# Optimization experiments

Measured on AMD Instinct MI355X. Metric: run time of the kernel, lower is better.

Reference implementation:

```python
import jax, jax.numpy as jnp
import numpy as np

EPS_MSG = 1e-7   # GENConv message epsilon
BN_EPS = 1e-5    # BatchNorm1d eps
NUM_GRAPHS = 1024


def _linear(x, W, b):
    return x @ W + b


def _batchnorm(x, gamma, beta):
    # training-mode batch statistics over the node dimension
    mu = jnp.mean(x, axis=0)
    var = jnp.mean((x - mu) ** 2, axis=0)
    return (x - mu) * jax.lax.rsqrt(var + BN_EPS) * gamma + beta


def _genconv(x, src, dst, e, t, W1, b1, gamma, beta, W2, b2, num_nodes):
    # message: relu(x_j + edge_attr) + eps, shape [E, H]
    msg = jax.nn.relu(x[src] + e) + EPS_MSG
    # learnable softmax aggregation over each destination's neighborhood
    s = msg * t
    m = jax.lax.stop_gradient(jax.ops.segment_max(s, dst, num_segments=num_nodes))
    m = jnp.where(jnp.isfinite(m), m, 0.0)
    ex = jnp.exp(s - m[dst])
    denom = jax.ops.segment_sum(ex, dst, num_segments=num_nodes)
    alpha = ex / (denom[dst] + 1e-16)
    agg = jax.ops.segment_sum(msg * alpha, dst, num_segments=num_nodes)  # [N, H]
    # GENConv MLP([H, 2H, H], norm='batch') applied to x + aggregated messages
    h = x + agg
    h = _linear(h, W1, b1)
    h = _batchnorm(h, gamma, beta)
    h = jax.nn.relu(h)
    return _linear(h, W2, b2)


def setup_inputs() -> dict:
    key = jax.random.key(0)
    N, E, FIN, FE, H, L, G, OUT = 50000, 1000000, 32, 16, 64, 4, NUM_GRAPHS, 1
    ks = jax.random.split(key, 32)

    def rn(k, shape, fan_in):
        return jax.random.normal(k, shape, dtype=jnp.float32) * (1.0 / np.sqrt(fan_in))

    inp = {}
    inp["x"] = jax.random.normal(ks[0], (N, FIN), dtype=jnp.float32)
    inp["edge_attr"] = jax.random.normal(ks[1], (E, FE), dtype=jnp.float32)
    inp["edge_index"] = jax.random.randint(ks[2], (2, E), 0, N)
    inp["batch"] = jnp.sort(jax.random.randint(ks[3], (N,), 0, G))
    # atom encoder: Linear(FIN,H) ReLU Linear(H,H) ReLU
    inp["atom_W1"] = rn(ks[4], (FIN, H), FIN); inp["atom_b1"] = jnp.zeros((H,), jnp.float32)
    inp["atom_W2"] = rn(ks[5], (H, H), H);     inp["atom_b2"] = jnp.zeros((H,), jnp.float32)
    # bond encoder: Linear(FE,H) ReLU Linear(H,H) ReLU
    inp["bond_W1"] = rn(ks[6], (FE, H), FE);   inp["bond_b1"] = jnp.zeros((H,), jnp.float32)
    inp["bond_W2"] = rn(ks[7], (H, H), H);     inp["bond_b2"] = jnp.zeros((H,), jnp.float32)
    # stacked GENConv params (L layers)
    inp["conv_t"] = jnp.ones((L,), jnp.float32)
    inp["conv_W1"] = rn(ks[8], (L, H, 2 * H), H)
    inp["conv_b1"] = jnp.zeros((L, 2 * H), jnp.float32)
    inp["conv_gamma"] = jnp.ones((L, 2 * H), jnp.float32)
    inp["conv_beta"] = jnp.zeros((L, 2 * H), jnp.float32)
    inp["conv_W2"] = rn(ks[9], (L, 2 * H, H), 2 * H)
    inp["conv_b2"] = jnp.zeros((L, H), jnp.float32)
    # head
    inp["lin1_W"] = rn(ks[10], (H, H), H);     inp["lin1_b"] = jnp.zeros((H,), jnp.float32)
    inp["lin2_W"] = rn(ks[11], (H, OUT), H);   inp["lin2_b"] = jnp.zeros((OUT,), jnp.float32)
    return inp


def reference(x, edge_attr, atom_W1, atom_b1, atom_W2, atom_b2,
              bond_W1, bond_b1, bond_W2, bond_b2,
              conv_t, conv_W1, conv_b1, conv_gamma, conv_beta, conv_W2, conv_b2,
              lin1_W, lin1_b, lin2_W, lin2_b,
              edge_index, batch):
    N = x.shape[0]
    src, dst = edge_index[0], edge_index[1]
    h = jax.nn.relu(_linear(jax.nn.relu(_linear(x, atom_W1, atom_b1)), atom_W2, atom_b2))
    e = jax.nn.relu(_linear(jax.nn.relu(_linear(edge_attr, bond_W1, bond_b1)), bond_W2, bond_b2))
    L = conv_t.shape[0]
    for i in range(L):
        h = _genconv(h, src, dst, e, conv_t[i], conv_W1[i], conv_b1[i],
                     conv_gamma[i], conv_beta[i], conv_W2[i], conv_b2[i], N)
        if i < L - 1:
            h = jax.nn.relu(h)
    g = jax.ops.segment_sum(h, batch, num_segments=NUM_GRAPHS)  # global_add_pool
    g = jax.nn.relu(_linear(g, lin1_W, lin1_b))
    return _linear(g, lin2_W, lin2_b)
```

## Files before the change

kernel.cpp:

```cpp
#include <hip/hip_runtime.h>
#include <hip/hip_bf16.h>
#include <math.h>

typedef __attribute__((ext_vector_type(8))) short bf16x8;
typedef __attribute__((ext_vector_type(4))) float f32x4;

__device__ inline unsigned f2bf(float f) {
    union { __hip_bfloat16 h; unsigned short u; } cv;
    cv.h = __float2bfloat16(f);
    return (unsigned)cv.u;
}
__device__ inline float bfu(unsigned u) {
    return __uint_as_float(u << 16);
}


__global__ void k_hist(const int* __restrict__ dst, int* __restrict__ counts, int E) {
    int e = blockIdx.x * blockDim.x + threadIdx.x;
    if (e < E) atomicAdd(&counts[dst[e]], 1);
}

__global__ void k_scan1(const int* __restrict__ counts, int* __restrict__ row_ptr,
                        int* __restrict__ csum, int n) {
    __shared__ int buf[1024];
    int tid = threadIdx.x;
    int base = blockIdx.x * 1024;
    int v = (base + tid < n) ? counts[base + tid] : 0;
    buf[tid] = v;
    __syncthreads();
    int inc = v;
    for (int off = 1; off < 1024; off <<= 1) {
        int add = (tid >= off) ? buf[tid - off] : 0;
        __syncthreads();
        inc += add;
        buf[tid] = inc;
        __syncthreads();
    }
    if (base + tid < n) row_ptr[base + tid] = inc - v;
    if (tid == 1023) csum[blockIdx.x] = inc;
}

__global__ void k_scan2(int* __restrict__ csum, int nc, int* __restrict__ total) {
    if (threadIdx.x == 0) {
        int run = 0;
        for (int i = 0; i < nc; ++i) { int c = csum[i]; csum[i] = run; run += c; }
        *total = run;
    }
}

__global__ void k_scan3(int* __restrict__ row_ptr, const int* __restrict__ csum,
                        const int* __restrict__ total, int n) {
    int i = blockIdx.x * blockDim.x + threadIdx.x;
    if (i < n) row_ptr[i] += csum[i >> 10];
    if (i == 0) row_ptr[n] = *total;
}

#define ECH 4096
__global__ __launch_bounds__(256) void k_scatter(const int* __restrict__ src,
                          const int* __restrict__ dst,
                          const int* __restrict__ row_ptr, int* __restrict__ fill,
                          int2* __restrict__ spe, int E, int NS) {
    int bs = blockIdx.x & 7;
    int chunk = blockIdx.x >> 3;
    int base = chunk * ECH;
    int lo = bs * NS, hi = lo + NS;
#pragma unroll 1
    for (int j = 0; j < ECH / 256; ++j) {
        int e = base + j * 256 + threadIdx.x;
        if (e < E) {
            int d = dst[e];
            if (d >= lo && d < hi) {
                int pos = row_ptr[d] + atomicAdd(&fill[d], 1);
                spe[pos] = make_int2(src[e], e);
            }
        }
    }
}

__global__ void k_gptr(const int* __restrict__ batch, int* __restrict__ gptr, int n, int G) {
    int i = blockIdx.x * blockDim.x + threadIdx.x;
    if (i > n) return;
    if (i == 0) {
        int b0 = batch[0];
        for (int g = 0; g <= b0; ++g) gptr[g] = 0;
    } else if (i == n) {
        int bl = batch[n - 1];
        for (int g = bl + 1; g <= G; ++g) gptr[g] = n;
    } else {
        int b = batch[i], pb = batch[i - 1];
        for (int g = pb + 1; g <= b; ++g) gptr[g] = i;
    }
}


__global__ void k_wt(const float* __restrict__ W1, const float* __restrict__ W2,
                     unsigned short* __restrict__ W1b, unsigned short* __restrict__ W2tb) {
    int tid = blockIdx.x * blockDim.x + threadIdx.x;
    if (tid < 1024) {
        int j = tid / 16, k = tid % 16;
        W1b[j * 16 + k] = (unsigned short)f2bf(W1[k * 64 + j]);
    }
    if (tid < 4096) {
        int j = tid / 64, k = tid % 64;
        W2tb[j * 64 + k] = (unsigned short)f2bf(W2[k * 64 + j]);
    }
}


#define TM 128
__global__ __launch_bounds__(256) void k_atom(const float* __restrict__ x,
        const float* __restrict__ W1, const float* __restrict__ b1,
        const float* __restrict__ W2, const float* __restrict__ b2,
        float* __restrict__ out, int M) {
    __shared__ float sU[TM * 65];
    __shared__ float sW1[32 * 64];
    __shared__ float sW2[64 * 64];
    __shared__ float sB1[64], sB2[64];
#define A_IN(r, c) sU[(r) * 33 + (c)]
#define A_T1(r, c) sU[(r) * 65 + (c)]
    int tid = threadIdx.x;
    int base = blockIdx.x * TM;
    for (int i = tid; i < 32 * 64 / 4; i += 256) ((float4*)sW1)[i] = ((const float4*)W1)[i];
    for (int i = tid; i < 64 * 64 / 4; i += 256) ((float4*)sW2)[i] = ((const float4*)W2)[i];
    if (tid < 64) { sB1[tid] = b1[tid]; sB2[tid] = b2[tid]; }
    for (int i = tid; i < TM * 32 / 4; i += 256) {
        int r = i / 8, c4 = i % 8;
        int row = base + r;
        float4 v = (row < M) ? ((const float4*)(x + (long)row * 32))[c4] : make_float4(0, 0, 0, 0);
        A_IN(r, c4 * 4 + 0) = v.x; A_IN(r, c4 * 4 + 1) = v.y;
        A_IN(r, c4 * 4 + 2) = v.z; A_IN(r, c4 * 4 + 3) = v.w;
    }
    __syncthreads();
    int r0 = (tid / 16) * 8;
    int c0 = (tid % 16) * 4;
    float acc[8][4];
#pragma unroll
    for (int i = 0; i < 8; i++)
#pragma unroll
        for (int j = 0; j < 4; j++) acc[i][j] = sB1[c0 + j];
    for (int k = 0; k < 32; k++) {
        float a[8], b[4];
#pragma unroll
        for (int i = 0; i < 8; i++) a[i] = A_IN(r0 + i, k);
#pragma unroll
        for (int j = 0; j < 4; j++) b[j] = sW1[k * 64 + c0 + j];
#pragma unroll
        for (int i = 0; i < 8; i++)
#pragma unroll
            for (int j = 0; j < 4; j++) acc[i][j] += a[i] * b[j];
    }
    __syncthreads();
#pragma unroll
    for (int i = 0; i < 8; i++)
#pragma unroll
        for (int j = 0; j < 4; j++) A_T1(r0 + i, c0 + j) = fmaxf(acc[i][j], 0.f);
    __syncthreads();
#pragma unroll
    for (int i = 0; i < 8; i++)
#pragma unroll
        for (int j = 0; j < 4; j++) acc[i][j] = sB2[c0 + j];
    for (int k = 0; k < 64; k++) {
        float a[8], b[4];
#pragma unroll
        for (int i = 0; i < 8; i++) a[i] = A_T1(r0 + i, k);
#pragma unroll
        for (int j = 0; j < 4; j++) b[j] = sW2[k * 64 + c0 + j];
#pragma unroll
        for (int i = 0; i < 8; i++)
#pragma unroll
            for (int j = 0; j < 4; j++) acc[i][j] += a[i] * b[j];
    }
#pragma unroll
    for (int i = 0; i < 8; i++) {
        int row = base + r0 + i;
        if (row < M) {
            float4 v = make_float4(fmaxf(acc[i][0], 0.f), fmaxf(acc[i][1], 0.f),
                                   fmaxf(acc[i][2], 0.f), fmaxf(acc[i][3], 0.f));
            *(float4*)(out + (long)row * 64 + c0) = v;
        }
    }
}


__global__ __launch_bounds__(256) void k_bond(const float* __restrict__ ea,
        const int2* __restrict__ spe,
        const unsigned short* __restrict__ W1b, const float* __restrict__ b1,
        const unsigned short* __restrict__ W2tb, const float* __restrict__ b2,
        unsigned short* __restrict__ e_q, int E) {
    __shared__ unsigned sT1[128 * 32];
    __shared__ unsigned sW2[64 * 32];
    int tid = threadIdx.x;

    for (int i = tid; i < 2048; i += 256) {
        int rw = i >> 5, cp = i & 31;
        sW2[rw * 32 + (cp ^ ((rw & 7) << 2))] = ((const unsigned*)W2tb)[i];
    }

    int wv = tid >> 6, lane = tid & 63;
    int lr = lane & 15, q = lane >> 4;

    union { bf16x8 v; uint4 u4; } bf1[4];
    float bias1[4];
#pragma unroll
    for (int nt = 0; nt < 4; ++nt) {
        bf1[nt].u4 = make_uint4(0, 0, 0, 0);
        if (q < 2)
            bf1[nt].u4 = *(const uint4*)(W1b + (nt * 16 + lr) * 16 + q * 8);
        bias1[nt] = b1[nt * 16 + lr];
    }

#pragma unroll
    for (int mt1 = 0; mt1 < 2; ++mt1) {
        int rtile = wv * 2 + mt1;
        long row1 = (long)blockIdx.x * 128 + rtile * 16 + lr;
        long eidx = row1 < (long)E ? row1 : (long)(E - 1);
        int eid = spe[eidx].y;
        union { bf16x8 v; uint4 u4; unsigned u[4]; } af1;
        af1.u4 = make_uint4(0, 0, 0, 0);
        if (q < 2) {
            const float4* er = (const float4*)(ea + (long)eid * 16 + q * 8);
            float4 u0 = er[0], u1 = er[1];
            af1.u[0] = f2bf(u0.x) | (f2bf(u0.y) << 16);
            af1.u[1] = f2bf(u0.z) | (f2bf(u0.w) << 16);
            af1.u[2] = f2bf(u1.x) | (f2bf(u1.y) << 16);
            af1.u[3] = f2bf(u1.z) | (f2bf(u1.w) << 16);
        }
#pragma unroll
        for (int nt = 0; nt < 4; ++nt) {
            f32x4 c0;
            c0[0] = bias1[nt]; c0[1] = bias1[nt]; c0[2] = bias1[nt]; c0[3] = bias1[nt];
            f32x4 d = __builtin_amdgcn_mfma_f32_16x16x32_bf16(af1.v, bf1[nt].v, c0, 0, 0, 0);
#pragma unroll
            for (int i = 0; i < 4; ++i) {
                unsigned hv = f2bf(fmaxf(d[i], 0.f));
                unsigned ov = (unsigned)__shfl_xor((int)hv, 1, 64);
                if ((lr & 1) == 0) {
                    int r = rtile * 16 + q * 4 + i;
                    int cp = nt * 8 + (lr >> 1);
                    sT1[r * 32 + (cp ^ ((r & 7) << 2))] = hv | (ov << 16);
                }
            }
        }
    }
    __syncthreads();

    bf16x8 bf[4][2];
#pragma unroll
    for (int nt = 0; nt < 4; ++nt)
#pragma unroll
        for (int ks = 0; ks < 2; ++ks) {
            int rw = nt * 16 + lr;
            int u = rw * 32 + ((ks * 16 + q * 4) ^ ((rw & 7) << 2));
            bf[nt][ks] = *(const bf16x8*)&sW2[u];
        }
    f32x4 acc[2][4];
#pragma unroll
    for (int mt = 0; mt < 2; ++mt)
#pragma unroll
        for (int nt = 0; nt < 4; ++nt) {
            float bias = b2[nt * 16 + lr];
            f32x4 c0; c0[0] = bias; c0[1] = bias; c0[2] = bias; c0[3] = bias;
            acc[mt][nt] = c0;
        }
#pragma unroll
    for (int mt = 0; mt < 2; ++mt) {
        int rw = (wv * 2 + mt) * 16 + lr;
#pragma unroll
        for (int ks = 0; ks < 2; ++ks) {
            int u = rw * 32 + ((ks * 16 + q * 4) ^ ((rw & 7) << 2));
            bf16x8 af = *(const bf16x8*)&sT1[u];
#pragma unroll
            for (int nt = 0; nt < 4; ++nt)
                acc[mt][nt] = __builtin_amdgcn_mfma_f32_16x16x32_bf16(
                    af, bf[nt][ks], acc[mt][nt], 0, 0, 0);
        }
    }
#pragma unroll
    for (int mt = 0; mt < 2; ++mt)
#pragma unroll
        for (int nt = 0; nt < 4; ++nt) {
            long r0 = (long)blockIdx.x * 128 + (wv * 2 + mt) * 16 + q * 4;
            unsigned p01 = f2bf(fmaxf(acc[mt][nt][0], 0.f)) |
                           (f2bf(fmaxf(acc[mt][nt][1], 0.f)) << 16);
            unsigned p23 = f2bf(fmaxf(acc[mt][nt][2], 0.f)) |
                           (f2bf(fmaxf(acc[mt][nt][3], 0.f)) << 16);
            long qb = ((r0 >> 2) * 64 + nt * 16 + lr) * 4;
            if (r0 + 3 < (long)E) {
                *(uint2*)(e_q + qb) = make_uint2(p01, p23);
            } else {
                unsigned vv[4] = {p01 & 0xffff, p01 >> 16, p23 & 0xffff, p23 >> 16};
#pragma unroll
                for (int i = 0; i < 4; ++i)
                    if (r0 + i < (long)E) e_q[qb + i] = (unsigned short)vv[i];
            }
        }
}


__global__ __launch_bounds__(256) void k_agg(const float* __restrict__ h,
        const unsigned short* __restrict__ e_q, const int2* __restrict__ spe,
        const int* __restrict__ row_ptr, const float* __restrict__ t_ptr, int layer,
        float* __restrict__ y, int n) {
    int wid = blockIdx.x * 4 + (threadIdx.x >> 6);
    int lane = threadIdx.x & 63;
    if (wid >= n) return;
    wid = __builtin_amdgcn_readfirstlane(wid);
    float tval = t_ptr[layer];
    int beg = row_ptr[wid], end = row_ptr[wid + 1];
    float m = -INFINITY, den = 0.f, num = 0.f;
    int i = beg;
    int astart = (beg + 3) & ~3; if (astart > end) astart = end;
    int aend = end & ~3;         if (aend < astart) aend = astart;
    for (; i < astart; ++i) {
        int s = spe[i].x;
        float ev = bfu((unsigned)e_q[((long)(i >> 2) * 64 + lane) * 4 + (i & 3)]);
        float hv = h[(long)s * 64 + lane];
        float msg = fmaxf(hv + ev, 0.f) + 1e-7f;
        float sv = msg * tval;
        float mn = fmaxf(m, sv);
        float sc = __expf(m - mn);
        float w = __expf(sv - mn);
        den = den * sc + w;
        num = num * sc + w * msg;
        m = mn;
    }
    for (; i < aend; i += 4) {
        int s0 = spe[i].x, s1 = spe[i + 1].x, s2 = spe[i + 2].x, s3 = spe[i + 3].x;
        uint2 ee = *(const uint2*)(e_q + ((long)(i >> 2) * 64 + lane) * 4);
        float ev0 = bfu(ee.x & 0xffff), ev1 = bfu(ee.x >> 16);
        float ev2 = bfu(ee.y & 0xffff), ev3 = bfu(ee.y >> 16);
        float hv0 = h[(long)s0 * 64 + lane];
        float hv1 = h[(long)s1 * 64 + lane];
        float hv2 = h[(long)s2 * 64 + lane];
        float hv3 = h[(long)s3 * 64 + lane];
        float msg0 = fmaxf(hv0 + ev0, 0.f) + 1e-7f;
        float msg1 = fmaxf(hv1 + ev1, 0.f) + 1e-7f;
        float msg2 = fmaxf(hv2 + ev2, 0.f) + 1e-7f;
        float msg3 = fmaxf(hv3 + ev3, 0.f) + 1e-7f;
        float sv0 = msg0 * tval, sv1 = msg1 * tval;
        float sv2 = msg2 * tval, sv3 = msg3 * tval;
        float mn = fmaxf(fmaxf(fmaxf(m, sv0), fmaxf(sv1, sv2)), sv3);
        float sc = __expf(m - mn);
        float w0 = __expf(sv0 - mn);
        float w1 = __expf(sv1 - mn);
        float w2 = __expf(sv2 - mn);
        float w3 = __expf(sv3 - mn);
        den = den * sc + ((w0 + w1) + (w2 + w3));
        num = num * sc + ((w0 * msg0 + w1 * msg1) + (w2 * msg2 + w3 * msg3));
        m = mn;
    }
    for (; i < end; ++i) {
        int s = spe[i].x;
        float ev = bfu((unsigned)e_q[((long)(i >> 2) * 64 + lane) * 4 + (i & 3)]);
        float hv = h[(long)s * 64 + lane];
        float msg = fmaxf(hv + ev, 0.f) + 1e-7f;
        float sv = msg * tval;
        float mn = fmaxf(m, sv);
        float sc = __expf(m - mn);
        float w = __expf(sv - mn);
        den = den * sc + w;
        num = num * sc + w * msg;
        m = mn;
    }
    float agg = (end > beg) ? num / (den + 1e-16f) : 0.f;
    y[(long)wid * 64 + lane] = h[(long)wid * 64 + lane] + agg;
}


__global__ __launch_bounds__(256) void k_gemm1(const float* __restrict__ y,
        const float* __restrict__ W1, const float* __restrict__ b1,
        float* __restrict__ h1, float* __restrict__ part, int n) {
    __shared__ float sA[64][65];
    __shared__ float sW[64 * 128];
    __shared__ float sB[128];
    __shared__ float sS[8][128];
    __shared__ float sS2[8][128];
    int tid = threadIdx.x;
    int base = blockIdx.x * 64;
    for (int i = tid; i < 64 * 128 / 4; i += 256) ((float4*)sW)[i] = ((const float4*)W1)[i];
    if (tid < 128) sB[tid] = b1[tid];
    for (int i = tid; i < 64 * 64 / 4; i += 256) {
        int r = i / 16, c4 = i % 16;
        int row = base + r;
        float4 v = (row < n) ? ((const float4*)(y + (long)row * 64))[c4] : make_float4(0, 0, 0, 0);
        sA[r][c4 * 4 + 0] = v.x; sA[r][c4 * 4 + 1] = v.y;
        sA[r][c4 * 4 + 2] = v.z; sA[r][c4 * 4 + 3] = v.w;
    }
    __syncthreads();
    int rg = tid / 32;
    int r0 = rg * 8;
    int c0 = (tid % 32) * 4;
    float acc[8][4];
#pragma unroll
    for (int i = 0; i < 8; i++)
#pragma unroll
        for (int j = 0; j < 4; j++) acc[i][j] = sB[c0 + j];
    for (int k = 0; k < 64; k++) {
        float a[8], b[4];
#pragma unroll
        for (int i = 0; i < 8; i++) a[i] = sA[r0 + i][k];
#pragma unroll
        for (int j = 0; j < 4; j++) b[j] = sW[k * 128 + c0 + j];
#pragma unroll
        for (int i = 0; i < 8; i++)
#pragma unroll
            for (int j = 0; j < 4; j++) acc[i][j] += a[i] * b[j];
    }
    float ps[4] = {0, 0, 0, 0}, ps2[4] = {0, 0, 0, 0};
#pragma unroll
    for (int i = 0; i < 8; i++) {
        int row = base + r0 + i;
        if (row < n) {
            float4 v = make_float4(acc[i][0], acc[i][1], acc[i][2], acc[i][3]);
            *(float4*)(h1 + (long)row * 128 + c0) = v;
#pragma unroll
            for (int j = 0; j < 4; j++) { ps[j] += acc[i][j]; ps2[j] += acc[i][j] * acc[i][j]; }
        }
    }
#pragma unroll
    for (int j = 0; j < 4; j++) { sS[rg][c0 + j] = ps[j]; sS2[rg][c0 + j] = ps2[j]; }
    __syncthreads();
    if (tid < 128) {
        float s = 0.f, s2 = 0.f;
#pragma unroll
        for (int g = 0; g < 8; g++) { s += sS[g][tid]; s2 += sS2[g][tid]; }
        part[blockIdx.x * 256 + tid] = s;
        part[blockIdx.x * 256 + 128 + tid] = s2;
    }
}


__global__ __launch_bounds__(256) void k_bnred(const float* __restrict__ part,
                                               float* __restrict__ part2, int nblk) {
    int c = threadIdx.x;
    int b = blockIdx.x;
    float s = 0.f;
    for (int r = b; r < nblk; r += 64) s += part[r * 256 + c];
    part2[b * 256 + c] = s;
}

__global__ __launch_bounds__(1024) void k_bnfin(const float* __restrict__ part2,
                        const float* __restrict__ gamma, const float* __restrict__ beta,
                        float* __restrict__ scale, float* __restrict__ shift, float invN) {
    __shared__ float red[4][256];
    __shared__ float tot[256];
    int c = threadIdx.x & 255;
    int g = threadIdx.x >> 8;
    float s = 0.f;
#pragma unroll
    for (int r = 0; r < 16; ++r) s += part2[(g * 16 + r) * 256 + c];
    red[g][c] = s;
    __syncthreads();
    if (threadIdx.x < 256) tot[c] = red[0][c] + red[1][c] + red[2][c] + red[3][c];
    __syncthreads();
    if (threadIdx.x < 128) {
        int cc = threadIdx.x;
        float mu = tot[cc] * invN;
        float var = fmaxf(tot[128 + cc] * invN - mu * mu, 0.f);
        float sc = gamma[cc] * rsqrtf(var + 1e-5f);
        scale[cc] = sc;
        shift[cc] = beta[cc] - mu * sc;
    }
}


__global__ __launch_bounds__(256) void k_gemm2(const float* __restrict__ h1,
        const float* __restrict__ scale, const float* __restrict__ shift,
        const float* __restrict__ W2, const float* __restrict__ b2,
        float* __restrict__ hout, int n, int dorelu) {
    __shared__ float sA[32][129];
    __shared__ float sW[128 * 64];
    __shared__ float sSc[128], sSh[128], sB[64];
    int tid = threadIdx.x;
    int base = blockIdx.x * 32;
    for (int i = tid; i < 128 * 64 / 4; i += 256) ((float4*)sW)[i] = ((const float4*)W2)[i];
    if (tid < 128) { sSc[tid] = scale[tid]; sSh[tid] = shift[tid]; }
    if (tid < 64) sB[tid] = b2[tid];
    __syncthreads();
    for (int i = tid; i < 32 * 128 / 4; i += 256) {
        int r = i / 32, c4 = i % 32;
        int row = base + r;
        float4 v = (row < n) ? ((const float4*)(h1 + (long)row * 128))[c4] : make_float4(0, 0, 0, 0);
        int c = c4 * 4;
        sA[r][c + 0] = fmaxf(v.x * sSc[c + 0] + sSh[c + 0], 0.f);
        sA[r][c + 1] = fmaxf(v.y * sSc[c + 1] + sSh[c + 1], 0.f);
        sA[r][c + 2] = fmaxf(v.z * sSc[c + 2] + sSh[c + 2], 0.f);
        sA[r][c + 3] = fmaxf(v.w * sSc[c + 3] + sSh[c + 3], 0.f);
    }
    __syncthreads();
    int r0 = (tid / 16) * 2;
    int c0 = (tid % 16) * 4;
    float acc[2][4];
#pragma unroll
    for (int i = 0; i < 2; i++)
#pragma unroll
        for (int j = 0; j < 4; j++) acc[i][j] = sB[c0 + j];
    for (int k = 0; k < 128; k++) {
        float a[2], b[4];
#pragma unroll
        for (int i = 0; i < 2; i++) a[i] = sA[r0 + i][k];
#pragma unroll
        for (int j = 0; j < 4; j++) b[j] = sW[k * 64 + c0 + j];
#pragma unroll
        for (int i = 0; i < 2; i++)
#pragma unroll
            for (int j = 0; j < 4; j++) acc[i][j] += a[i] * b[j];
    }
#pragma unroll
    for (int i = 0; i < 2; i++) {
        int row = base + r0 + i;
        if (row < n) {
            float4 v;
            v.x = dorelu ? fmaxf(acc[i][0], 0.f) : acc[i][0];
            v.y = dorelu ? fmaxf(acc[i][1], 0.f) : acc[i][1];
            v.z = dorelu ? fmaxf(acc[i][2], 0.f) : acc[i][2];
            v.w = dorelu ? fmaxf(acc[i][3], 0.f) : acc[i][3];
            *(float4*)(hout + (long)row * 64 + c0) = v;
        }
    }
}


__global__ __launch_bounds__(64) void k_head(const float* __restrict__ h,
        const int* __restrict__ gptr,
        const float* __restrict__ W1, const float* __restrict__ b1,
        const float* __restrict__ W2, const float* __restrict__ b2,
        float* __restrict__ out) {
    int g = blockIdx.x;
    int lane = threadIdx.x;
    int beg = gptr[g], end = gptr[g + 1];
    float s = 0.f;
    for (int r = beg; r < end; ++r) s += h[(long)r * 64 + lane];
    __shared__ float sg[64];
    sg[lane] = s;
    __syncthreads();
    float acc = b1[lane];
    for (int k = 0; k < 64; k++) acc += sg[k] * W1[k * 64 + lane];
    acc = fmaxf(acc, 0.f);
    float v = acc * W2[lane];
#pragma unroll
    for (int off = 32; off > 0; off >>= 1) v += __shfl_down(v, off, 64);
    if (lane == 0) out[g] = v + b2[0];
}


extern "C" void kernel_launch(void* const* d_in, const int* in_sizes, int n_in,
                              void* d_out, int out_size, void* d_ws, size_t ws_size,
                              hipStream_t stream) {
    const float* x      = (const float*)d_in[0];
    const float* ea     = (const float*)d_in[1];
    const int*   ei     = (const int*)d_in[2];
    const int*   batch  = (const int*)d_in[3];
    const float* atomW1 = (const float*)d_in[4];
    const float* atomb1 = (const float*)d_in[5];
    const float* atomW2 = (const float*)d_in[6];
    const float* atomb2 = (const float*)d_in[7];
    const float* bondW1 = (const float*)d_in[8];
    const float* bondb1 = (const float*)d_in[9];
    const float* bondW2 = (const float*)d_in[10];
    const float* bondb2 = (const float*)d_in[11];
    const float* convT  = (const float*)d_in[12];
    const float* convW1 = (const float*)d_in[13];
    const float* convb1 = (const float*)d_in[14];
    const float* convG  = (const float*)d_in[15];
    const float* convBt = (const float*)d_in[16];
    const float* convW2 = (const float*)d_in[17];
    const float* convb2 = (const float*)d_in[18];
    const float* lin1W  = (const float*)d_in[19];
    const float* lin1b  = (const float*)d_in[20];
    const float* lin2W  = (const float*)d_in[21];
    const float* lin2b  = (const float*)d_in[22];
    float* out = (float*)d_out;

    const int N = in_sizes[0] / 32;
    const int E = in_sizes[1] / 16;
    const int G = out_size;
    const int Lconv = in_sizes[12];
    const int nchunk = (N + 1023) / 1024;
    const int nblk1 = (N + 63) / 64;
    const int NS = (N + 7) / 8;
    const int nchE = (E + ECH - 1) / ECH;
    const size_t nquad = (size_t)((E + 3) / 4);

    size_t need = 0;
    auto count = [&](size_t bytes) { need += (bytes + 255) & ~(size_t)255; };
    count(nquad * 4 * 64 * 2);
    count((size_t)N * 64 * 4);
    count((size_t)N * 64 * 4);
    count((size_t)N * 128 * 4);
    count((size_t)E * 8);
    count((size_t)(N + 1) * 4);
    count((size_t)N * 4);
    count((size_t)N * 4);
    count((size_t)(G + 1) * 4);
    count((size_t)nblk1 * 256 * 4);
    count((size_t)64 * 256 * 4);
    count(128 * 4); count(128 * 4);
    count((size_t)(nchunk + 1) * 4);
    count(4);
    count(1024 * 2);
    count(4096 * 2);
    if (ws_size < need) {
        hipMemsetAsync(d_out, 0, (size_t)out_size * 4, stream);
        return;
    }

    char* ws = (char*)d_ws;
    size_t off = 0;
    auto alloc = [&](size_t bytes) -> void* {
        void* p = ws + off;
        off += (bytes + 255) & ~(size_t)255;
        return p;
    };
    unsigned short* e_q = (unsigned short*)alloc(nquad * 4 * 64 * 2);
    float* h_cur    = (float*)alloc((size_t)N * 64 * 4);
    float* y_buf    = (float*)alloc((size_t)N * 64 * 4);
    float* h1       = (float*)alloc((size_t)N * 128 * 4);
    int2*  spe      = (int2*)alloc((size_t)E * 8);
    int*   row_ptr  = (int*)alloc((size_t)(N + 1) * 4);
    int*   counts   = (int*)alloc((size_t)N * 4);
    int*   fill     = (int*)alloc((size_t)N * 4);
    int*   gptr     = (int*)alloc((size_t)(G + 1) * 4);
    float* part     = (float*)alloc((size_t)nblk1 * 256 * 4);
    float* part2    = (float*)alloc((size_t)64 * 256 * 4);
    float* bnscale  = (float*)alloc(128 * 4);
    float* bnshift  = (float*)alloc(128 * 4);
    int*   csum     = (int*)alloc((size_t)(nchunk + 1) * 4);
    int*   totalp   = (int*)alloc(4);
    unsigned short* W1b  = (unsigned short*)alloc(1024 * 2);
    unsigned short* W2tb = (unsigned short*)alloc(4096 * 2);
    (void)n_in;

    hipMemsetAsync(counts, 0, (size_t)N * 4, stream);
    hipMemsetAsync(fill, 0, (size_t)N * 4, stream);

    const int* src = ei;
    const int* dst = ei + E;

    k_hist<<<(E + 255) / 256, 256, 0, stream>>>(dst, counts, E);
    k_scan1<<<nchunk, 1024, 0, stream>>>(counts, row_ptr, csum, N);
    k_scan2<<<1, 64, 0, stream>>>(csum, nchunk, totalp);
    k_scan3<<<(N + 255) / 256, 256, 0, stream>>>(row_ptr, csum, totalp, N);
    k_scatter<<<nchE * 8, 256, 0, stream>>>(src, dst, row_ptr, fill, spe, E, NS);
    k_gptr<<<(N + 256) / 256, 256, 0, stream>>>(batch, gptr, N, G);
    k_wt<<<16, 256, 0, stream>>>(bondW1, bondW2, W1b, W2tb);

    k_atom<<<(N + TM - 1) / TM, 256, 0, stream>>>(x, atomW1, atomb1, atomW2, atomb2, h_cur, N);
    k_bond<<<(E + 127) / 128, 256, 0, stream>>>(ea, spe, W1b, bondb1, W2tb, bondb2, e_q, E);

    for (int l = 0; l < Lconv; ++l) {
        k_agg<<<(N + 3) / 4, 256, 0, stream>>>(h_cur, e_q, spe, row_ptr, convT, l, y_buf, N);
        k_gemm1<<<nblk1, 256, 0, stream>>>(y_buf, convW1 + (size_t)l * 64 * 128,
                                           convb1 + (size_t)l * 128, h1, part, N);
        k_bnred<<<64, 256, 0, stream>>>(part, part2, nblk1);
        k_bnfin<<<1, 1024, 0, stream>>>(part2, convG + (size_t)l * 128, convBt + (size_t)l * 128,
                                        bnscale, bnshift, 1.0f / (float)N);
        k_gemm2<<<(N + 31) / 32, 256, 0, stream>>>(h1, bnscale, bnshift,
                                                   convW2 + (size_t)l * 128 * 64,
                                                   convb2 + (size_t)l * 64, h_cur, N,
                                                   (l < Lconv - 1) ? 1 : 0);
    }

    k_head<<<G, 64, 0, stream>>>(h_cur, gptr, lin1W, lin1b, lin2W, lin2b, out);
}
```

Measured before the change: 656.5 us.

## Gather bf16 copy of node features in aggregation and unroll edge loop by eight

The atom encoder and the second GEMM now also write a bf16 copy of the node features. The aggregation kernel gathers from that copy instead of the fp32 array, which halves the bytes of the random per-edge gather. The main edge loop is also unrolled to process eight edges per iteration, putting more independent loads in flight. This costs an extra write pass per layer and lowers the precision of the gathered features, while the self term still comes from fp32.

```diff
diff --git a/kernel.cpp b/kernel.cpp
--- a/kernel.cpp
+++ b/kernel.cpp
@@ -111,7 +111,7 @@
 __global__ __launch_bounds__(256) void k_atom(const float* __restrict__ x,
         const float* __restrict__ W1, const float* __restrict__ b1,
         const float* __restrict__ W2, const float* __restrict__ b2,
-        float* __restrict__ out, int M) {
+        float* __restrict__ out, unsigned short* __restrict__ hb, int M) {
     __shared__ float sU[TM * 65];
     __shared__ float sW1[32 * 64];
     __shared__ float sW2[64 * 64];
@@ -177,6 +177,9 @@
             float4 v = make_float4(fmaxf(acc[i][0], 0.f), fmaxf(acc[i][1], 0.f),
                                    fmaxf(acc[i][2], 0.f), fmaxf(acc[i][3], 0.f));
             *(float4*)(out + (long)row * 64 + c0) = v;
+            unsigned p01 = f2bf(v.x) | (f2bf(v.y) << 16);
+            unsigned p23 = f2bf(v.z) | (f2bf(v.w) << 16);
+            *(uint2*)(hb + (long)row * 64 + c0) = make_uint2(p01, p23);
         }
     }
 }
@@ -298,6 +301,7 @@
 
 
 __global__ __launch_bounds__(256) void k_agg(const float* __restrict__ h,
+        const unsigned short* __restrict__ h_bf,
         const unsigned short* __restrict__ e_q, const int2* __restrict__ spe,
         const int* __restrict__ row_ptr, const float* __restrict__ t_ptr, int layer,
         float* __restrict__ y, int n) {
@@ -314,7 +318,7 @@
     for (; i < astart; ++i) {
         int s = spe[i].x;
         float ev = bfu((unsigned)e_q[((long)(i >> 2) * 64 + lane) * 4 + (i & 3)]);
-        float hv = h[(long)s * 64 + lane];
+        float hv = bfu((unsigned)h_bf[(long)s * 64 + lane]);
         float msg = fmaxf(hv + ev, 0.f) + 1e-7f;
         float sv = msg * tval;
         float mn = fmaxf(m, sv);
@@ -324,19 +328,52 @@
         num = num * sc + w * msg;
         m = mn;
     }
+    for (; i + 8 <= aend; i += 8) {
+        int s0 = spe[i].x,     s1 = spe[i + 1].x, s2 = spe[i + 2].x, s3 = spe[i + 3].x;
+        int s4 = spe[i + 4].x, s5 = spe[i + 5].x, s6 = spe[i + 6].x, s7 = spe[i + 7].x;
+        uint2 ea0 = *(const uint2*)(e_q + ((long)(i >> 2) * 64 + lane) * 4);
+        uint2 ea1 = *(const uint2*)(e_q + ((long)((i >> 2) + 1) * 64 + lane) * 4);
+        float hv0 = bfu((unsigned)h_bf[(long)s0 * 64 + lane]);
+        float hv1 = bfu((unsigned)h_bf[(long)s1 * 64 + lane]);
+        float hv2 = bfu((unsigned)h_bf[(long)s2 * 64 + lane]);
+        float hv3 = bfu((unsigned)h_bf[(long)s3 * 64 + lane]);
+        float hv4 = bfu((unsigned)h_bf[(long)s4 * 64 + lane]);
+        float hv5 = bfu((unsigned)h_bf[(long)s5 * 64 + lane]);
+        float hv6 = bfu((unsigned)h_bf[(long)s6 * 64 + lane]);
+        float hv7 = bfu((unsigned)h_bf[(long)s7 * 64 + lane]);
+        float msg0 = fmaxf(hv0 + bfu(ea0.x & 0xffff), 0.f) + 1e-7f;
+        float msg1 = fmaxf(hv1 + bfu(ea0.x >> 16), 0.f) + 1e-7f;
+        float msg2 = fmaxf(hv2 + bfu(ea0.y & 0xffff), 0.f) + 1e-7f;
+        float msg3 = fmaxf(hv3 + bfu(ea0.y >> 16), 0.f) + 1e-7f;
+        float msg4 = fmaxf(hv4 + bfu(ea1.x & 0xffff), 0.f) + 1e-7f;
+        float msg5 = fmaxf(hv5 + bfu(ea1.x >> 16), 0.f) + 1e-7f;
+        float msg6 = fmaxf(hv6 + bfu(ea1.y & 0xffff), 0.f) + 1e-7f;
+        float msg7 = fmaxf(hv7 + bfu(ea1.y >> 16), 0.f) + 1e-7f;
+        float sv0 = msg0 * tval, sv1 = msg1 * tval, sv2 = msg2 * tval, sv3 = msg3 * tval;
+        float sv4 = msg4 * tval, sv5 = msg5 * tval, sv6 = msg6 * tval, sv7 = msg7 * tval;
+        float mn = fmaxf(fmaxf(fmaxf(fmaxf(m, sv0), fmaxf(sv1, sv2)),
+                               fmaxf(fmaxf(sv3, sv4), fmaxf(sv5, sv6))), sv7);
+        float sc = __expf(m - mn);
+        float w0 = __expf(sv0 - mn), w1 = __expf(sv1 - mn);
+        float w2 = __expf(sv2 - mn), w3 = __expf(sv3 - mn);
+        float w4 = __expf(sv4 - mn), w5 = __expf(sv5 - mn);
+        float w6 = __expf(sv6 - mn), w7 = __expf(sv7 - mn);
+        den = den * sc + (((w0 + w1) + (w2 + w3)) + ((w4 + w5) + (w6 + w7)));
+        num = num * sc + (((w0 * msg0 + w1 * msg1) + (w2 * msg2 + w3 * msg3)) +
+                          ((w4 * msg4 + w5 * msg5) + (w6 * msg6 + w7 * msg7)));
+        m = mn;
+    }
     for (; i < aend; i += 4) {
         int s0 = spe[i].x, s1 = spe[i + 1].x, s2 = spe[i + 2].x, s3 = spe[i + 3].x;
         uint2 ee = *(const uint2*)(e_q + ((long)(i >> 2) * 64 + lane) * 4);
-        float ev0 = bfu(ee.x & 0xffff), ev1 = bfu(ee.x >> 16);
-        float ev2 = bfu(ee.y & 0xffff), ev3 = bfu(ee.y >> 16);
-        float hv0 = h[(long)s0 * 64 + lane];
-        float hv1 = h[(long)s1 * 64 + lane];
-        float hv2 = h[(long)s2 * 64 + lane];
-        float hv3 = h[(long)s3 * 64 + lane];
-        float msg0 = fmaxf(hv0 + ev0, 0.f) + 1e-7f;
-        float msg1 = fmaxf(hv1 + ev1, 0.f) + 1e-7f;
-        float msg2 = fmaxf(hv2 + ev2, 0.f) + 1e-7f;
-        float msg3 = fmaxf(hv3 + ev3, 0.f) + 1e-7f;
+        float hv0 = bfu((unsigned)h_bf[(long)s0 * 64 + lane]);
+        float hv1 = bfu((unsigned)h_bf[(long)s1 * 64 + lane]);
+        float hv2 = bfu((unsigned)h_bf[(long)s2 * 64 + lane]);
+        float hv3 = bfu((unsigned)h_bf[(long)s3 * 64 + lane]);
+        float msg0 = fmaxf(hv0 + bfu(ee.x & 0xffff), 0.f) + 1e-7f;
+        float msg1 = fmaxf(hv1 + bfu(ee.x >> 16), 0.f) + 1e-7f;
+        float msg2 = fmaxf(hv2 + bfu(ee.y & 0xffff), 0.f) + 1e-7f;
+        float msg3 = fmaxf(hv3 + bfu(ee.y >> 16), 0.f) + 1e-7f;
         float sv0 = msg0 * tval, sv1 = msg1 * tval;
         float sv2 = msg2 * tval, sv3 = msg3 * tval;
         float mn = fmaxf(fmaxf(fmaxf(m, sv0), fmaxf(sv1, sv2)), sv3);
@@ -352,7 +389,7 @@
     for (; i < end; ++i) {
         int s = spe[i].x;
         float ev = bfu((unsigned)e_q[((long)(i >> 2) * 64 + lane) * 4 + (i & 3)]);
-        float hv = h[(long)s * 64 + lane];
+        float hv = bfu((unsigned)h_bf[(long)s * 64 + lane]);
         float msg = fmaxf(hv + ev, 0.f) + 1e-7f;
         float sv = msg * tval;
         float mn = fmaxf(m, sv);
@@ -467,7 +504,7 @@
 __global__ __launch_bounds__(256) void k_gemm2(const float* __restrict__ h1,
         const float* __restrict__ scale, const float* __restrict__ shift,
         const float* __restrict__ W2, const float* __restrict__ b2,
-        float* __restrict__ hout, int n, int dorelu) {
+        float* __restrict__ hout, unsigned short* __restrict__ hb, int n, int dorelu) {
     __shared__ float sA[32][129];
     __shared__ float sW[128 * 64];
     __shared__ float sSc[128], sSh[128], sB[64];
@@ -516,6 +553,11 @@
             v.z = dorelu ? fmaxf(acc[i][2], 0.f) : acc[i][2];
             v.w = dorelu ? fmaxf(acc[i][3], 0.f) : acc[i][3];
             *(float4*)(hout + (long)row * 64 + c0) = v;
+            if (dorelu) {
+                unsigned p01 = f2bf(v.x) | (f2bf(v.y) << 16);
+                unsigned p23 = f2bf(v.z) | (f2bf(v.w) << 16);
+                *(uint2*)(hb + (long)row * 64 + c0) = make_uint2(p01, p23);
+            }
         }
     }
 }
@@ -586,6 +628,7 @@
     auto count = [&](size_t bytes) { need += (bytes + 255) & ~(size_t)255; };
     count(nquad * 4 * 64 * 2);
     count((size_t)N * 64 * 4);
+    count((size_t)N * 64 * 2);
     count((size_t)N * 64 * 4);
     count((size_t)N * 128 * 4);
     count((size_t)E * 8);
@@ -614,6 +657,7 @@
     };
     unsigned short* e_q = (unsigned short*)alloc(nquad * 4 * 64 * 2);
     float* h_cur    = (float*)alloc((size_t)N * 64 * 4);
+    unsigned short* h_bf = (unsigned short*)alloc((size_t)N * 64 * 2);
     float* y_buf    = (float*)alloc((size_t)N * 64 * 4);
     float* h1       = (float*)alloc((size_t)N * 128 * 4);
     int2*  spe      = (int2*)alloc((size_t)E * 8);
@@ -645,11 +689,13 @@
     k_gptr<<<(N + 256) / 256, 256, 0, stream>>>(batch, gptr, N, G);
     k_wt<<<16, 256, 0, stream>>>(bondW1, bondW2, W1b, W2tb);
 
-    k_atom<<<(N + TM - 1) / TM, 256, 0, stream>>>(x, atomW1, atomb1, atomW2, atomb2, h_cur, N);
+    k_atom<<<(N + TM - 1) / TM, 256, 0, stream>>>(x, atomW1, atomb1, atomW2, atomb2,
+                                                  h_cur, h_bf, N);
     k_bond<<<(E + 127) / 128, 256, 0, stream>>>(ea, spe, W1b, bondb1, W2tb, bondb2, e_q, E);
 
     for (int l = 0; l < Lconv; ++l) {
-        k_agg<<<(N + 3) / 4, 256, 0, stream>>>(h_cur, e_q, spe, row_ptr, convT, l, y_buf, N);
+        k_agg<<<(N + 3) / 4, 256, 0, stream>>>(h_cur, h_bf, e_q, spe, row_ptr, convT, l,
+                                               y_buf, N);
         k_gemm1<<<nblk1, 256, 0, stream>>>(y_buf, convW1 + (size_t)l * 64 * 128,
                                            convb1 + (size_t)l * 128, h1, part, N);
         k_bnred<<<64, 256, 0, stream>>>(part, part2, nblk1);
@@ -657,7 +703,7 @@
                                         bnscale, bnshift, 1.0f / (float)N);
         k_gemm2<<<(N + 31) / 32, 256, 0, stream>>>(h1, bnscale, bnshift,
                                                    convW2 + (size_t)l * 128 * 64,
-                                                   convb2 + (size_t)l * 64, h_cur, N,
+                                                   convb2 + (size_t)l * 64, h_cur, h_bf, N,
                                                    (l < Lconv - 1) ? 1 : 0);
     }
 
```

After: 611.2 us. 1.07x faster.
